# Kernel tuning notes

Measured on AMD Instinct MI355X. Metric: run time of the kernel, lower is better.

## Reference

```python
import jax, jax.numpy as jnp
import numpy as np

S, T, B = 50, 50, 64
SRC_V, TRG_V = 36616, 23262
E, EH, DH = 300, 512, 1024


def setup_inputs() -> dict:
    key = jax.random.key(0)
    ks = jax.random.split(key, 20)
    n = lambda k, shape: jax.random.normal(k, shape, jnp.float32) * 0.05
    return {
        "train_src_batch": jax.random.randint(ks[0], (S, B), 0, SRC_V),
        "train_trg_batch": jax.random.randint(ks[1], (T, B), 0, TRG_V),
        "emb_en": n(ks[2], (SRC_V, E)),
        "emb_de": n(ks[3], (TRG_V, E)),
        "enc_W_ih_f": n(ks[4], (4 * EH, E)),
        "enc_W_hh_f": n(ks[5], (4 * EH, EH)),
        "enc_b_f": n(ks[6], (4 * EH,)),
        "enc_W_ih_b": n(ks[7], (4 * EH, E)),
        "enc_W_hh_b": n(ks[8], (4 * EH, EH)),
        "enc_b_b": n(ks[9], (4 * EH,)),
        "dec_W_ih": n(ks[10], (4 * DH, E + DH)),
        "dec_W_hh": n(ks[11], (4 * DH, DH)),
        "dec_b": n(ks[12], (4 * DH,)),
        "W_gen": n(ks[13], (TRG_V, DH)),
        "b_gen": n(ks[14], (TRG_V,)),
        "W_i": n(ks[15], (DH, DH)),
        "W_o": n(ks[16], (DH, 2 * DH)),
    }


def _lstm_step(x, h, c, W_ih, W_hh, b):
    # PyTorch gate order: i, f, g, o
    gates = x @ W_ih.T + h @ W_hh.T + b
    i, f, g, o = jnp.split(gates, 4, axis=-1)
    c_new = jax.nn.sigmoid(f) * c + jax.nn.sigmoid(i) * jnp.tanh(g)
    h_new = jax.nn.sigmoid(o) * jnp.tanh(c_new)
    return h_new, c_new


def _run_lstm(x_seq, W_ih, W_hh, b, hidden):
    h0 = jnp.zeros((x_seq.shape[1], hidden), x_seq.dtype)
    def step(carry, x):
        h, c = carry
        h, c = _lstm_step(x, h, c, W_ih, W_hh, b)
        return (h, c), h
    (h, c), hs = jax.lax.scan(step, (h0, h0), x_seq)
    return hs, h, c


def _forward(train_src_batch, train_trg_batch, emb_en, emb_de,
             enc_W_ih_f, enc_W_hh_f, enc_b_f, enc_W_ih_b, enc_W_hh_b, enc_b_b,
             dec_W_ih, dec_W_hh, dec_b, W_gen, b_gen, W_i, W_o):
    x = emb_en[train_src_batch]                       # [S,B,E]
    hs_f, hf, cf = _run_lstm(x, enc_W_ih_f, enc_W_hh_f, enc_b_f, EH)
    hs_b, hb, cb = _run_lstm(x[::-1], enc_W_ih_b, enc_W_hh_b, enc_b_b, EH)
    output_hs = jnp.concatenate([hs_f, hs_b[::-1]], axis=-1)  # [S,B,1024]
    # Faithful to h.contiguous().view(B,1024) on direction-major [2,B,512]
    h = jnp.reshape(jnp.stack([hf, hb], axis=0), (B, DH))
    c = jnp.reshape(jnp.stack([cf, cb], axis=0), (B, DH))

    emb_trg = emb_de[train_trg_batch[: T - 1]]        # [T-1,B,E]

    def step(carry, e):
        h, c = carry
        # score[j,b] = output_hs[j,b] . (W_i h[b])  (the diag of the original mm)
        scores = jnp.einsum('sbd,bd->sb', output_hs, h @ W_i.T)
        # legacy nn.Softmax() on 2D input -> softmax over dim=1 (batch axis)
        a = jax.nn.softmax(scores, axis=1)
        s_t = jnp.einsum('sb,sbd->bd', a, output_hs)
        c_t = jnp.tanh(jnp.concatenate([s_t, h], axis=1) @ W_o.T)
        dec_in = jnp.concatenate([c_t, e], axis=1)    # [B, 1024+300]
        h, c = _lstm_step(dec_in, h, c, dec_W_ih, dec_W_hh, dec_b)
        logp = jax.nn.log_softmax(h @ W_gen.T + b_gen, axis=1)
        return (h, c), logp

    _, outs = jax.lax.scan(step, (h, c), emb_trg)     # [T-1,B,V]
    out0 = jnp.zeros((1, B, TRG_V), outs.dtype)       # output[0] filled with 0
    return jnp.concatenate([out0, outs], axis=0)      # [T,B,V]


def reference(train_src_batch, train_trg_batch, emb_en, emb_de,
              enc_W_ih_f, enc_W_hh_f, enc_b_f, enc_W_ih_b, enc_W_hh_b, enc_b_b,
              dec_W_ih, dec_W_hh, dec_b, W_gen, b_gen, W_i, W_o):
    return _forward(train_src_batch, train_trg_batch, emb_en, emb_de,
                    enc_W_ih_f, enc_W_hh_f, enc_b_f, enc_W_ih_b, enc_W_hh_b, enc_b_b,
                    dec_W_ih, dec_W_hh, dec_b, W_gen, b_gen, W_i, W_o)
```

## Files before the change

kernel.cpp:

```cpp
#include <hip/hip_runtime.h>
#include <hip/hip_bf16.h>

#define SS 50
#define TT 50
#define BB 64
#define TRGV 23262
#define EE 300
#define EH 512
#define DH 1024

#define GMRE 3136
#define GMP 3200
#define GK 1024
#define GNRE TRGV
#define GNP 23296

typedef short bf16x8 __attribute__((ext_vector_type(8)));
typedef float f32x4 __attribute__((ext_vector_type(4)));

__device__ __forceinline__ void glds16(const void* g, void* l) {
  __builtin_amdgcn_global_load_lds(
      (const __attribute__((address_space(1))) void*)g,
      (__attribute__((address_space(3))) void*)l, 16, 0, 0);
}

__device__ __forceinline__ float sigm(float x) { return 1.f / (1.f + expf(-x)); }
__device__ __forceinline__ float sum4(f32x4 v) { return v[0] + v[1] + v[2] + v[3]; }

__device__ __forceinline__ void split2(float x, __hip_bfloat16& hi, __hip_bfloat16& lo) {
  hi = __float2bfloat16(x);
  lo = __float2bfloat16(x - __bfloat162float(hi));
}

__device__ __forceinline__ void gbarg(unsigned* arrive, unsigned* gen,
                                      int idxInGrp, int n, bool poller) {
  __syncthreads();
  unsigned g = __hip_atomic_load(gen, __ATOMIC_RELAXED, __HIP_MEMORY_SCOPE_AGENT);
  if (threadIdx.x == 0)
    __hip_atomic_store(arrive + idxInGrp, g + 1u, __ATOMIC_RELEASE, __HIP_MEMORY_SCOPE_AGENT);
  if (poller) {
    int i = threadIdx.x;
    if (i < n) {
      while (__hip_atomic_load(arrive + i, __ATOMIC_RELAXED, __HIP_MEMORY_SCOPE_AGENT) < g + 1u)
        __builtin_amdgcn_s_sleep(1);
      (void)__hip_atomic_load(arrive + i, __ATOMIC_ACQUIRE, __HIP_MEMORY_SCOPE_AGENT);
    }
    __syncthreads();
    if (threadIdx.x == 0)
      __hip_atomic_store(gen, g + 1u, __ATOMIC_RELEASE, __HIP_MEMORY_SCOPE_AGENT);
  }
  if (threadIdx.x == 0) {
    while (__hip_atomic_load(gen, __ATOMIC_RELAXED, __HIP_MEMORY_SCOPE_AGENT) < g + 1u)
      __builtin_amdgcn_s_sleep(1);
    (void)__hip_atomic_load(gen, __ATOMIC_ACQUIRE, __HIP_MEMORY_SCOPE_AGENT);
  }
  __syncthreads();
}

__global__ void k_zero(float* __restrict__ p, long n) {
  long i = (long)blockIdx.x * 256 + threadIdx.x;
  if (i < n) p[i] = 0.f;
}
__global__ void k_zero_bf(__hip_bfloat16* __restrict__ p, long n) {
  long i = (long)blockIdx.x * 256 + threadIdx.x;
  if (i < n) p[i] = __float2bfloat16(0.f);
}

__global__ void k_embed(const int* __restrict__ src, const float* __restrict__ emb,
                        float* __restrict__ x) {
  int id = blockIdx.x * 256 + threadIdx.x;
  if (id >= SS * BB * EE) return;
  int sb = id / EE, e = id % EE;
  x[id] = emb[(long)src[sb] * EE + e];
}

__global__ void k_dbperm(const float* __restrict__ db, float* __restrict__ dbp) {
  int id = blockIdx.x * 256 + threadIdx.x;
  if (id >= 4096) return;
  int u = id >> 2, g = id & 3;
  dbp[id] = db[g * 1024 + u];
}

__global__ void k_split_pad(const float* __restrict__ in, int ld_in, int col_off,
                            int Kreal, int Kpad, int rows_real, long rows_pad,
                            int mode, __hip_bfloat16* __restrict__ out) {
  long id = (long)blockIdx.x * 256 + threadIdx.x;
  if (id >= rows_pad * Kpad) return;
  long r = id / Kpad;
  int k = id % Kpad;
  float v = 0.f;
  if (r < rows_real && k < Kreal) {
    if (mode == 3) {
      v = in[(long)k * ld_in + col_off + r];
    } else {
      long sr = r;
      if (mode == 1) sr = ((49 - (r >> 6)) << 6) + (r & 63);
      else if (mode == 2) sr = (long)(r & 3) * 1024 + (r >> 2);
      v = in[sr * ld_in + col_off + k];
    }
  }
  __hip_bfloat16 hi, lo;
  split2(v, hi, lo);
  out[r * 2 * Kpad + k] = hi;
  out[r * 2 * Kpad + Kpad + k] = lo;
}

__global__ void k_embgather_split(const int* __restrict__ trg, const float* __restrict__ emb,
                                  __hip_bfloat16* __restrict__ out) {
  long id = (long)blockIdx.x * 256 + threadIdx.x;
  if (id >= 3200L * 320) return;
  long r = id / 320;
  int k = id % 320;
  int t = r >> 6, b = r & 63;
  float v = 0.f;
  if (t < TT - 1 && k < EE) v = emb[(long)trg[t * BB + b] * EE + k];
  __hip_bfloat16 hi, lo;
  split2(v, hi, lo);
  out[r * 640 + k] = hi;
  out[r * 640 + 320 + k] = lo;
}

__global__ void k_tobf16_pad(const float* __restrict__ W, __hip_bfloat16* __restrict__ Wb,
                             long nrow_real, long nrow_pad, int K) {
  long id = (long)blockIdx.x * 256 + threadIdx.x;
  if (id >= nrow_pad * K) return;
  long r = id / K;
  Wb[id] = __float2bfloat16(r < nrow_real ? W[id] : 0.f);
}

__global__ void k_repackT(const float* __restrict__ in, float* __restrict__ out) {
  long id = (long)blockIdx.x * 256 + threadIdx.x;
  if (id >= 3200L * 1024) return;
  long r = id >> 10;
  int n = id & 1023;
  out[((long)(n >> 2) * 3200 + r) * 4 + (n & 3)] = in[id];
}

__global__ void k_repackG(const float* __restrict__ in, float* __restrict__ out) {
  long id = (long)blockIdx.x * 256 + threadIdx.x;
  if (id >= 3200L * 1024) return;
  long b = id / 51200;
  long r = id % 51200;
  long s = r >> 10;
  int d = r & 1023;
  out[id] = in[((long)s * 64 + b) * 1024 + d];
}

template<int OUTBF>
__global__ __launch_bounds__(256) void k_gsplit(
    const __hip_bfloat16* __restrict__ A2, const __hip_bfloat16* __restrict__ W2,
    const float* __restrict__ bias, void* __restrict__ Cout,
    int Mreal, int Nreal, int ldc, int Kpad) {
  __shared__ __hip_bfloat16 As[128 * 32];
  __shared__ __hip_bfloat16 Bs[128 * 32];
  int tid = threadIdx.x, lane = tid & 63, w = tid >> 6;
  long m0 = (long)blockIdx.y * 128, n0 = (long)blockIdx.x * 128;
  int lda2 = 2 * Kpad;
  int srow = lane >> 2;
  int scol = (lane & 3) * 8;
  char* lA0 = (char*)As + w * 2048;
  char* lA1 = lA0 + 1024;
  char* lB0 = (char*)Bs + w * 2048;
  char* lB1 = lB0 + 1024;
  int wm = (w >> 1) * 64, wn = (w & 1) * 64;
  int fr = lane & 15;
  int kc = (lane >> 4) * 8;
  f32x4 acc[4][4] = {};

  for (int seg = 0; seg < 3; ++seg) {
    const __hip_bfloat16* Ab = A2 + (seg == 1 ? Kpad : 0);
    const __hip_bfloat16* Wb = W2 + (seg == 2 ? Kpad : 0);
    const __hip_bfloat16* gA0 = Ab + (m0 + w * 32 + srow) * (long)lda2 + scol;
    const __hip_bfloat16* gA1 = gA0 + 16L * lda2;
    const __hip_bfloat16* gB0 = Wb + (n0 + w * 32 + srow) * (long)lda2 + scol;
    const __hip_bfloat16* gB1 = gB0 + 16L * lda2;
    for (int kt = 0; kt < Kpad / 32; ++kt) {
      int k0 = kt * 32;
      glds16(gA0 + k0, lA0);
      glds16(gA1 + k0, lA1);
      glds16(gB0 + k0, lB0);
      glds16(gB1 + k0, lB1);
      __syncthreads();
      bf16x8 a[4], b[4];
      for (int mi = 0; mi < 4; ++mi)
        a[mi] = *(const bf16x8*)(As + (wm + mi * 16 + fr) * 32 + kc);
      for (int ni = 0; ni < 4; ++ni)
        b[ni] = *(const bf16x8*)(Bs + (wn + ni * 16 + fr) * 32 + kc);
      for (int mi = 0; mi < 4; ++mi)
        for (int ni = 0; ni < 4; ++ni)
          acc[mi][ni] = __builtin_amdgcn_mfma_f32_16x16x32_bf16(a[mi], b[ni], acc[mi][ni], 0, 0, 0);
      __syncthreads();
    }
  }

  for (int mi = 0; mi < 4; ++mi) {
    for (int ni = 0; ni < 4; ++ni) {
      int n = (int)n0 + wn + ni * 16 + (lane & 15);
      if (n >= Nreal) continue;
      float bv = bias ? bias[n] : 0.f;
      for (int r = 0; r < 4; ++r) {
        int m = (int)m0 + wm + mi * 16 + (lane >> 4) * 4 + r;
        if (m >= Mreal) continue;
        float v = acc[mi][ni][r] + bv;
        if (OUTBF) ((__hip_bfloat16*)Cout)[(long)m * ldc + n] = __float2bfloat16(v);
        else ((float*)Cout)[(long)m * ldc + n] = v;
      }
    }
  }
}

__global__ __launch_bounds__(512) void persist_enc(
    const float* __restrict__ xW_f, const float* __restrict__ xW_b,
    const float* __restrict__ Whf, const float* __restrict__ Whb,
    float* __restrict__ hs, float* hA, float* hB, float* hA2, float* hB2,
    float* __restrict__ cf, float* __restrict__ cb,
    float* __restrict__ hd0, float* __restrict__ hT0, float* __restrict__ cdD,
    __hip_bfloat16* __restrict__ x2A, unsigned* __restrict__ bar) {
  __shared__ float WL[16 * 516];
  int t = threadIdx.x;
  int blk = blockIdx.x;
  int dir = blk >> 7, bl = blk & 127;
  const float* Whh = dir ? Whb : Whf;
  const float* xWb0 = dir ? xW_b : xW_f;
  float* c = dir ? cb : cf;
  float* hp = dir ? hA2 : hA;
  float* hn = dir ? hB2 : hB;
  unsigned* arrG = bar + dir * 128;
  unsigned* genG = bar + 784 + dir * 16;
  unsigned* arrA = bar + 256;
  unsigned* genA = bar + 816;

  for (int idx = t; idx < 16 * 512; idx += 512) {
    int r = idx >> 9, k = idx & 511;
    int srcrow = (r & 3) * 512 + (bl * 4 + (r >> 2));
    WL[r * 516 + k] = Whh[(long)srcrow * 512 + k];
  }
  __syncthreads();

  int j = t & 15;
  int b0 = t >> 4, b1 = b0 + 32;
  int g = j & 3;
  int ju = bl * 4 + (j >> 2);
  int lbase = (t & 63) & ~3;
  const f32x4* wq = (const f32x4*)(WL + j * 516);

  for (int s = 0; s < SS; ++s) {
    const f32x4* h0q = (const f32x4*)(hp + b0 * 512);
    const f32x4* h1q = (const f32x4*)(hp + b1 * 512);
    f32x4 v0 = {0, 0, 0, 0}, v1 = {0, 0, 0, 0};
    for (int q = 0; q < 128; ++q) {
      f32x4 wv = wq[q];
      v0 += wv * h0q[q];
      v1 += wv * h1q[q];
    }
    const float* xW = xWb0 + (long)(s * BB) * 2048;
    float a0 = sum4(v0) + xW[b0 * 2048 + g * 512 + ju];
    float a1 = sum4(v1) + xW[b1 * 2048 + g * 512 + ju];
    float gi0 = __shfl(a0, lbase + 0), gf0 = __shfl(a0, lbase + 1);
    float gg0 = __shfl(a0, lbase + 2), go0 = __shfl(a0, lbase + 3);
    float gi1 = __shfl(a1, lbase + 0), gf1 = __shfl(a1, lbase + 1);
    float gg1 = __shfl(a1, lbase + 2), go1 = __shfl(a1, lbase + 3);
    if ((t & 3) == 0) {
      int hscol = dir ? (512 + ju) : ju;
      int srow = dir ? (SS - 1 - s) : s;
      long hsrow0 = (long)(srow * BB + b0) * DH + hscol;
      long hsrow1 = (long)(srow * BB + b1) * DH + hscol;
      float cn0 = sigm(gf0) * c[b0 * 512 + ju] + sigm(gi0) * tanhf(gg0);
      float hn0 = sigm(go0) * tanhf(cn0);
      c[b0 * 512 + ju] = cn0;
      hn[b0 * 512 + ju] = hn0;
      hs[hsrow0] = hn0;
      float cn1 = sigm(gf1) * c[b1 * 512 + ju] + sigm(gi1) * tanhf(gg1);
      float hn1 = sigm(go1) * tanhf(cn1);
      c[b1 * 512 + ju] = cn1;
      hn[b1 * 512 + ju] = hn1;
      hs[hsrow1] = hn1;
    }
    float* tmp = hp; hp = hn; hn = tmp;
    gbarg(arrG, genG, bl, 128, bl == 0);
  }
  gbarg(arrA, genA, blk, 256, blk == 0);
  int gid = blk * 512 + t;
  if (gid < 65536) {
    int d2 = gid >> 15, b = (gid >> 9) & 63, j2 = gid & 511;
    float hv = (d2 ? hA2 : hA)[b * 512 + j2];
    float cv = (d2 ? cb : cf)[b * 512 + j2];
    hd0[gid] = hv;
    cdD[gid] = cv;
    int bp = gid >> 10, jp = gid & 1023;
    hT0[jp * 64 + bp] = hv;
    __hip_bfloat16 hi, lo;
    split2(hv, hi, lo);
    x2A[bp * 4096 + 1024 + jp] = hi;
    x2A[bp * 4096 + 3072 + jp] = lo;
  }
}

__global__ __launch_bounds__(1024) void persist_dec(
    const float* __restrict__ Gb, const float* __restrict__ HsWo1T,
    const float* __restrict__ Wo, const float* __restrict__ dWih,
    const float* __restrict__ dWhh, const __hip_bfloat16* __restrict__ Eg,
    float* hd0, float* hd1, float* hT0, float* hT1,
    float* __restrict__ cd, float* __restrict__ scoresG,
    __hip_bfloat16* __restrict__ A_bf,
    __hip_bfloat16* __restrict__ xA, __hip_bfloat16* __restrict__ xB,
    unsigned* __restrict__ bar) {
  __shared__ __hip_bfloat16 WB[16 * 4096];
  __shared__ float Abuf[4096];
  int t = threadIdx.x;
  int blk = blockIdx.x;
  int w = t >> 6, lane = t & 63;
  unsigned* arrive = bar + 512;
  unsigned* gen = bar + 832;

  for (int idx = t; idx < 16 * 2048; idx += 1024) {
    int jj = idx >> 11;
    int k = idx & 2047;
    int rp2 = blk * 16 + jj;
    long srcrow = (long)(rp2 & 3) * 1024 + (rp2 >> 2);
    float v = (k < 1024) ? dWih[srcrow * 1324 + k] : dWhh[srcrow * 1024 + (k - 1024)];
    __hip_bfloat16 hi, lo;
    split2(v, hi, lo);
    WB[((k >> 3) * 16 + jj) * 8 + (k & 7)] = hi;
    WB[(((k + 2048) >> 3) * 16 + jj) * 8 + (k & 7)] = lo;
  }
  __syncthreads();

  float* hcur = hd0; float* hnew = hd1;
  float* hTc = hT0;  float* hTn = hT1;
  int j = t & 15, b = t >> 4;
  int rp = blk * 16 + j;
  int ju = blk * 4 + (j >> 2);
  int lbase = (t & 63) & ~3;
  const f32x4* hw4 = (const f32x4*)(HsWo1T + (long)blk * 3200 * 4);
  f32x4* Abuf4 = (f32x4*)Abuf;
  int mt = w & 3, kg = w >> 2;
  int row_a = mt * 16 + (lane & 15), kq = lane >> 4;
  int s_ks = t >> 8, s_kq = (t >> 6) & 3, s_row = t & 63;
  const float* wo2 = Wo + (long)(blk * 4) * 2048 + 1024;

  for (int ts = 0; ts < TT - 1; ++ts) {
    const __hip_bfloat16* xc = (ts & 1) ? xB : xA;
    __hip_bfloat16* xn = (ts & 1) ? xA : xB;
    float eg = __bfloat162float(Eg[((long)(ts * BB + b)) * 4096 + rp]);

    if (blk < BB) {
      int sp = t >> 4, cc = t & 15;
      if (sp < SS) {
        const f32x4* gq = (const f32x4*)(Gb + (long)blk * 51200 + sp * 1024 + cc * 64);
        const f32x4* hq = (const f32x4*)(hcur + blk * DH + cc * 64);
        f32x4 a4 = {0, 0, 0, 0};
        #pragma unroll
        for (int q = 0; q < 16; ++q) a4 += gq[q] * hq[q];
        float p = sum4(a4);
        p += __shfl_xor(p, 1);
        p += __shfl_xor(p, 2);
        p += __shfl_xor(p, 4);
        p += __shfl_xor(p, 8);
        if (cc == 0) scoresG[sp * 64 + blk] = p;
      }
    }
    {
      f32x4 z1 = {0, 0, 0, 0};
      for (int k = w * 64; k < w * 64 + 64; ++k) {
        float hb = hTc[k * 64 + lane];
        f32x4 wv = {wo2[k], wo2[2048 + k], wo2[4096 + k], wo2[6144 + k]};
        z1 += hb * wv;
      }
      Abuf4[w * 64 + lane] = z1;
    }
    gbarg(arrive, gen, blk, 256, blk == 0);

    {
      f32x4 z2 = {0, 0, 0, 0};
      for (int s = w; s < SS; s += 16) {
        float sc = scoresG[s * 64 + lane];
        float m = sc;
        for (int o = 32; o > 0; o >>= 1) m = fmaxf(m, __shfl_xor(m, o));
        float e = expf(sc - m);
        float su = e;
        for (int o = 32; o > 0; o >>= 1) su += __shfl_xor(su, o);
        z2 += (e / su) * hw4[s * 64 + lane];
      }
      Abuf4[w * 64 + lane] += z2;
      __syncthreads();
      if (t < 256) {
        int bb = t >> 2, nl = t & 3;
        float sv = 0.f;
        for (int i = 0; i < 16; ++i) sv += Abuf[(i * 64 + bb) * 4 + nl];
        float ct = tanhf(sv);
        __hip_bfloat16 hi, lo;
        split2(ct, hi, lo);
        xn = xn;
        ((__hip_bfloat16*)xc)[bb * 4096 + blk * 4 + nl] = hi;
        ((__hip_bfloat16*)xc)[bb * 4096 + 2048 + blk * 4 + nl] = lo;
      }
    }
    gbarg(arrive, gen, blk, 256, blk == 0);

    {
      f32x4 acc = {0, 0, 0, 0};
      for (int seg = 0; seg < 3; ++seg) {
        int aoff = (seg == 1) ? 2048 : 0;
        int woff = (seg == 2) ? 2048 : 0;
        for (int c = 0; c < 16; ++c) {
          int k0 = c * 128;
          glds16(xc + (long)s_row * 4096 + aoff + k0 + s_ks * 32 + s_kq * 8,
                 (char*)Abuf + t * 16);
          __syncthreads();
          bf16x8 a = *(const bf16x8*)((__hip_bfloat16*)Abuf + kg * 2048 + kq * 512 + row_a * 8);
          int gidx = ((woff + k0 + kg * 32) >> 3) + kq;
          bf16x8 bfr = *(const bf16x8*)(WB + gidx * 128 + (lane & 15) * 8);
          acc = __builtin_amdgcn_mfma_f32_16x16x32_bf16(a, bfr, acc, 0, 0, 0);
          __syncthreads();
        }
      }
      for (int r = 0; r < 4; ++r) {
        int row = mt * 16 + kq * 4 + r;
        Abuf[kg * 1024 + row * 16 + (lane & 15)] = acc[r];
      }
      __syncthreads();
      float gv = Abuf[t] + Abuf[1024 + t] + Abuf[2048 + t] + Abuf[3072 + t] + eg;
      float gi0 = __shfl(gv, lbase + 0), gf0 = __shfl(gv, lbase + 1);
      float gg0 = __shfl(gv, lbase + 2), go0 = __shfl(gv, lbase + 3);
      if ((t & 3) == 0) {
        float cn0 = sigm(gf0) * cd[b * DH + ju] + sigm(gi0) * tanhf(gg0);
        float hn0 = sigm(go0) * tanhf(cn0);
        cd[b * DH + ju] = cn0;
        hnew[b * DH + ju] = hn0;
        hTn[ju * 64 + b] = hn0;
        __hip_bfloat16 hi, lo;
        split2(hn0, hi, lo);
        A_bf[(long)ts * (BB * DH) + b * DH + ju] = hi;
        xn[b * 4096 + 1024 + ju] = hi;
        xn[b * 4096 + 3072 + ju] = lo;
      }
    }
    { float* x = hcur; hcur = hnew; hnew = x; }
    { float* x = hTc; hTc = hTn; hTn = x; }
    gbarg(arrive, gen, blk, 256, blk == 0);
  }
}

__global__ __launch_bounds__(256) void k_gen_mfma(
    const __hip_bfloat16* __restrict__ A, const __hip_bfloat16* __restrict__ Bw,
    const float* __restrict__ bias, float* __restrict__ C) {
  __shared__ __hip_bfloat16 As[128 * 32];
  __shared__ __hip_bfloat16 Bs[128 * 32];
  int tid = threadIdx.x;
  int lane = tid & 63, w = tid >> 6;
  long m0 = (long)blockIdx.y * 128, n0 = (long)blockIdx.x * 128;
  int srow = lane >> 2;
  int scol = (lane & 3) * 8;
  const __hip_bfloat16* gA0 = A + (m0 + w * 32 + srow) * GK + scol;
  const __hip_bfloat16* gA1 = gA0 + 16 * GK;
  const __hip_bfloat16* gB0 = Bw + (n0 + w * 32 + srow) * GK + scol;
  const __hip_bfloat16* gB1 = gB0 + 16 * GK;
  char* lA0 = (char*)As + w * 2048;
  char* lA1 = lA0 + 1024;
  char* lB0 = (char*)Bs + w * 2048;
  char* lB1 = lB0 + 1024;
  int wm = (w >> 1) * 64, wn = (w & 1) * 64;
  int fr = lane & 15;
  int kc = (lane >> 4) * 8;
  f32x4 acc[4][4] = {};
  for (int kt = 0; kt < GK / 32; ++kt) {
    int k0 = kt * 32;
    glds16(gA0 + k0, lA0);
    glds16(gA1 + k0, lA1);
    glds16(gB0 + k0, lB0);
    glds16(gB1 + k0, lB1);
    __syncthreads();
    bf16x8 a[4], b[4];
    for (int mi = 0; mi < 4; ++mi)
      a[mi] = *(const bf16x8*)(As + (wm + mi * 16 + fr) * 32 + kc);
    for (int ni = 0; ni < 4; ++ni)
      b[ni] = *(const bf16x8*)(Bs + (wn + ni * 16 + fr) * 32 + kc);
    for (int mi = 0; mi < 4; ++mi)
      for (int ni = 0; ni < 4; ++ni)
        acc[mi][ni] = __builtin_amdgcn_mfma_f32_16x16x32_bf16(a[mi], b[ni], acc[mi][ni], 0, 0, 0);
    __syncthreads();
  }
  for (int mi = 0; mi < 4; ++mi) {
    for (int ni = 0; ni < 4; ++ni) {
      int n = (int)n0 + wn + ni * 16 + (lane & 15);
      if (n >= GNRE) continue;
      float bv = bias[n];
      for (int r = 0; r < 4; ++r) {
        int m = (int)m0 + wm + mi * 16 + (lane >> 4) * 4 + r;
        if (m < GMRE) C[(long)m * TRGV + n] = acc[mi][ni][r] + bv;
      }
    }
  }
}

__global__ __launch_bounds__(256) void k_logsoftmax(float* __restrict__ out) {
  int r = blockIdx.x;
  float* p = out + (long)(BB + r) * TRGV;
  int tid = threadIdx.x;
  __shared__ float red[256];
  float m = -1e30f;
  for (int i = tid; i < TRGV; i += 256) m = fmaxf(m, p[i]);
  red[tid] = m;
  __syncthreads();
  for (int s = 128; s > 0; s >>= 1) {
    if (tid < s) red[tid] = fmaxf(red[tid], red[tid + s]);
    __syncthreads();
  }
  m = red[0];
  __syncthreads();
  float sum = 0.f;
  for (int i = tid; i < TRGV; i += 256) sum += expf(p[i] - m);
  red[tid] = sum;
  __syncthreads();
  for (int s = 128; s > 0; s >>= 1) {
    if (tid < s) red[tid] += red[tid + s];
    __syncthreads();
  }
  float lse = m + logf(red[0]);
  for (int i = tid; i < TRGV; i += 256) p[i] -= lse;
}

extern "C" void kernel_launch(void* const* d_in, const int* in_sizes, int n_in,
                              void* d_out, int out_size, void* d_ws, size_t ws_size,
                              hipStream_t stream) {
  const int* src = (const int*)d_in[0];
  const int* trg = (const int*)d_in[1];
  const float* emb_en = (const float*)d_in[2];
  const float* emb_de = (const float*)d_in[3];
  const float* eWih_f = (const float*)d_in[4];
  const float* eWhh_f = (const float*)d_in[5];
  const float* eb_f = (const float*)d_in[6];
  const float* eWih_b = (const float*)d_in[7];
  const float* eWhh_b = (const float*)d_in[8];
  const float* eb_b = (const float*)d_in[9];
  const float* dWih = (const float*)d_in[10];
  const float* dWhh = (const float*)d_in[11];
  const float* db = (const float*)d_in[12];
  const float* Wgen = (const float*)d_in[13];
  const float* bgen = (const float*)d_in[14];
  const float* Wi = (const float*)d_in[15];
  const float* Wo = (const float*)d_in[16];
  float* out = (float*)d_out;

  float* base = (float*)d_ws;
  __hip_bfloat16* xsf = (__hip_bfloat16*)base;
  __hip_bfloat16* xsb = (__hip_bfloat16*)(base + 1024000);
  __hip_bfloat16* Wihf2 = (__hip_bfloat16*)(base + 2048000);
  __hip_bfloat16* Wihb2 = (__hip_bfloat16*)(base + 2703360);
  float* xW_f = base + 3358720;
  float* xW_b = base + 9912320;
  __hip_bfloat16* hs2 = (__hip_bfloat16*)base;
  __hip_bfloat16* Wi2 = (__hip_bfloat16*)(base + 3276800);
  __hip_bfloat16* Wo12 = (__hip_bfloat16*)(base + 4325376);
  __hip_bfloat16* eg2 = (__hip_bfloat16*)(base + 5373952);
  __hip_bfloat16* Wce2 = (__hip_bfloat16*)(base + 6397952);
  __hip_bfloat16* E_g = (__hip_bfloat16*)(base + 7708672);
  __hip_bfloat16* Wgen_bf = (__hip_bfloat16*)base;
  float* p = base + 16465920;
  float* x_enc = p; p += SS * BB * EE;
  float* hs = p; p += (long)SS * BB * DH;
  float* G = p; p += (long)SS * BB * DH;
  float* Gb = p; p += (long)SS * BB * DH;
  float* HsWo1 = p; p += (long)SS * BB * DH;
  float* HsWo1T = p; p += (long)SS * BB * DH;
  __hip_bfloat16* A_bf = (__hip_bfloat16*)p; p += (GMP * GK) / 2;
  __hip_bfloat16* x2A = (__hip_bfloat16*)p; p += (BB * 4096) / 2;
  __hip_bfloat16* x2B = (__hip_bfloat16*)p; p += (BB * 4096) / 2;
  float* dbp = p; p += 4096;
  float* scoresG = p; p += SS * BB;
  float* hd0 = p; p += BB * DH;
  float* hd1 = p; p += BB * DH;
  float* hT0 = p; p += BB * DH;
  float* hT1 = p; p += BB * DH;
  float* cd = p; p += BB * DH;
  float* hA = p; p += BB * EH;
  float* hB = p; p += BB * EH;
  float* hA2 = p; p += BB * EH;
  float* hB2 = p; p += BB * EH;
  float* cf = p; p += BB * EH;
  float* cb = p; p += BB * EH;
  unsigned* bar = (unsigned*)p; p += 1024;

  dim3 b256(256);

  k_embed<<<dim3((SS * BB * EE + 255) / 256), b256, 0, stream>>>(src, emb_en, x_enc);
  k_zero<<<dim3((6 * BB * EH + 255) / 256), b256, 0, stream>>>(hA, 6 * BB * EH);
  k_zero<<<dim3(4), b256, 0, stream>>>((float*)bar, 1024);
  k_zero<<<dim3((int)(((long)BB * TRGV + 255) / 256)), b256, 0, stream>>>(out, (long)BB * TRGV);
  k_zero_bf<<<dim3(((GMP - GMRE) * GK + 255) / 256), b256, 0, stream>>>(
      A_bf + (long)GMRE * GK, (long)(GMP - GMRE) * GK);
  k_dbperm<<<dim3(16), b256, 0, stream>>>(db, dbp);

  k_split_pad<<<dim3((3200 * 320 + 255) / 256), b256, 0, stream>>>(
      x_enc, EE, 0, EE, 320, 3200, 3200, 0, xsf);
  k_split_pad<<<dim3((3200 * 320 + 255) / 256), b256, 0, stream>>>(
      x_enc, EE, 0, EE, 320, 3200, 3200, 1, xsb);
  k_split_pad<<<dim3((2048 * 320 + 255) / 256), b256, 0, stream>>>(
      eWih_f, EE, 0, EE, 320, 2048, 2048, 0, Wihf2);
  k_split_pad<<<dim3((2048 * 320 + 255) / 256), b256, 0, stream>>>(
      eWih_b, EE, 0, EE, 320, 2048, 2048, 0, Wihb2);
  k_gsplit<0><<<dim3(16, 25), b256, 0, stream>>>(xsf, Wihf2, eb_f, xW_f, 3200, 2048, 2048, 320);
  k_gsplit<0><<<dim3(16, 25), b256, 0, stream>>>(xsb, Wihb2, eb_b, xW_b, 3200, 2048, 2048, 320);

  {
    void* args[] = {(void*)&xW_f, (void*)&xW_b, (void*)&eWhh_f, (void*)&eWhh_b,
                    (void*)&hs, (void*)&hA, (void*)&hB, (void*)&hA2, (void*)&hB2,
                    (void*)&cf, (void*)&cb, (void*)&hd0, (void*)&hT0, (void*)&cd,
                    (void*)&x2A, (void*)&bar};
    hipLaunchCooperativeKernel((const void*)persist_enc, dim3(256), dim3(512),
                               args, 0, stream);
  }

  k_split_pad<<<dim3((int)((3200L * 1024 + 255) / 256)), b256, 0, stream>>>(
      hs, DH, 0, DH, 1024, 3200, 3200, 0, hs2);
  k_split_pad<<<dim3((int)((1024L * 1024 + 255) / 256)), b256, 0, stream>>>(
      Wi, DH, 0, DH, 1024, 1024, 1024, 3, Wi2);
  k_split_pad<<<dim3((int)((1024L * 1024 + 255) / 256)), b256, 0, stream>>>(
      Wo, 2 * DH, 0, DH, 1024, 1024, 1024, 0, Wo12);
  k_embgather_split<<<dim3((int)((3200L * 320 + 255) / 256)), b256, 0, stream>>>(
      trg, emb_de, eg2);
  k_split_pad<<<dim3((int)((4096L * 320 + 255) / 256)), b256, 0, stream>>>(
      dWih, 1324, 1024, EE, 320, 4096, 4096, 2, Wce2);
  k_gsplit<0><<<dim3(8, 25), b256, 0, stream>>>(hs2, Wi2, (const float*)nullptr, G, 3200, 1024, 1024, 1024);
  k_gsplit<0><<<dim3(8, 25), b256, 0, stream>>>(hs2, Wo12, (const float*)nullptr, HsWo1, 3200, 1024, 1024, 1024);
  k_repackG<<<dim3((int)((3200L * 1024 + 255) / 256)), b256, 0, stream>>>(G, Gb);
  k_repackT<<<dim3((int)((3200L * 1024 + 255) / 256)), b256, 0, stream>>>(HsWo1, HsWo1T);
  k_gsplit<1><<<dim3(32, 25), b256, 0, stream>>>(eg2, Wce2, dbp, E_g, 3136, 4096, 4096, 320);

  {
    void* args[] = {(void*)&Gb, (void*)&HsWo1T, (void*)&Wo, (void*)&dWih, (void*)&dWhh,
                    (void*)&E_g, (void*)&hd0, (void*)&hd1, (void*)&hT0, (void*)&hT1,
                    (void*)&cd, (void*)&scoresG, (void*)&A_bf, (void*)&x2A, (void*)&x2B,
                    (void*)&bar};
    hipLaunchCooperativeKernel((const void*)persist_dec, dim3(256), dim3(1024),
                               args, 0, stream);
  }

  k_tobf16_pad<<<dim3((int)(((long)GNP * GK + 255) / 256)), b256, 0, stream>>>(
      Wgen, Wgen_bf, GNRE, GNP, GK);
  k_gen_mfma<<<dim3(GNP / 128, GMP / 128), b256, 0, stream>>>(
      A_bf, Wgen_bf, bgen, out + (long)BB * TRGV);
  k_logsoftmax<<<dim3((TT - 1) * BB), b256, 0, stream>>>(out);
}
```

Measured before the change: 6.669 ms.

## Pad barrier slots, spread attention scores over 200 blocks, drop LDS staging in decoder GEMV

Barrier arrival counters are spaced 16 words apart so each block's flag sits on its own cache line, and the poller becomes the last block instead of block 0. Attention scores are now computed by 200 blocks, one wave per (s,b) pair, reading G directly, which removes the separate repackG kernel and its buffer. The decoder gate MFMA loop reads A fragments straight from global memory rather than staging them through LDS with two __syncthreads per chunk. The aim is to shorten the per-step critical path of the persistent decoder. The cost is uncoalesced-looking direct global A loads that depend on cache hits, and a larger barrier buffer.

```diff
diff --git a/kernel.cpp b/kernel.cpp
--- a/kernel.cpp
+++ b/kernel.cpp
@@ -37,13 +37,13 @@
   __syncthreads();
   unsigned g = __hip_atomic_load(gen, __ATOMIC_RELAXED, __HIP_MEMORY_SCOPE_AGENT);
   if (threadIdx.x == 0)
-    __hip_atomic_store(arrive + idxInGrp, g + 1u, __ATOMIC_RELEASE, __HIP_MEMORY_SCOPE_AGENT);
+    __hip_atomic_store(arrive + idxInGrp * 16, g + 1u, __ATOMIC_RELEASE, __HIP_MEMORY_SCOPE_AGENT);
   if (poller) {
     int i = threadIdx.x;
     if (i < n) {
-      while (__hip_atomic_load(arrive + i, __ATOMIC_RELAXED, __HIP_MEMORY_SCOPE_AGENT) < g + 1u)
+      while (__hip_atomic_load(arrive + i * 16, __ATOMIC_RELAXED, __HIP_MEMORY_SCOPE_AGENT) < g + 1u)
         __builtin_amdgcn_s_sleep(1);
-      (void)__hip_atomic_load(arrive + i, __ATOMIC_ACQUIRE, __HIP_MEMORY_SCOPE_AGENT);
+      (void)__hip_atomic_load(arrive + i * 16, __ATOMIC_ACQUIRE, __HIP_MEMORY_SCOPE_AGENT);
     }
     __syncthreads();
     if (threadIdx.x == 0)
@@ -134,16 +134,6 @@
   long r = id >> 10;
   int n = id & 1023;
   out[((long)(n >> 2) * 3200 + r) * 4 + (n & 3)] = in[id];
-}
-
-__global__ void k_repackG(const float* __restrict__ in, float* __restrict__ out) {
-  long id = (long)blockIdx.x * 256 + threadIdx.x;
-  if (id >= 3200L * 1024) return;
-  long b = id / 51200;
-  long r = id % 51200;
-  long s = r >> 10;
-  int d = r & 1023;
-  out[id] = in[((long)s * 64 + b) * 1024 + d];
 }
 
 template<int OUTBF>
@@ -225,10 +215,10 @@
   float* c = dir ? cb : cf;
   float* hp = dir ? hA2 : hA;
   float* hn = dir ? hB2 : hB;
-  unsigned* arrG = bar + dir * 128;
-  unsigned* genG = bar + 784 + dir * 16;
-  unsigned* arrA = bar + 256;
-  unsigned* genA = bar + 816;
+  unsigned* arrG = bar + dir * 2048;
+  unsigned* genG = bar + 12288 + dir * 16;
+  unsigned* arrA = bar + 4096;
+  unsigned* genA = bar + 12320;
 
   for (int idx = t; idx < 16 * 512; idx += 512) {
     int r = idx >> 9, k = idx & 511;
@@ -297,7 +287,7 @@
 }
 
 __global__ __launch_bounds__(1024) void persist_dec(
-    const float* __restrict__ Gb, const float* __restrict__ HsWo1T,
+    const float* __restrict__ G, const float* __restrict__ HsWo1T,
     const float* __restrict__ Wo, const float* __restrict__ dWih,
     const float* __restrict__ dWhh, const __hip_bfloat16* __restrict__ Eg,
     float* hd0, float* hd1, float* hT0, float* hT1,
@@ -305,13 +295,14 @@
     __hip_bfloat16* __restrict__ A_bf,
     __hip_bfloat16* __restrict__ xA, __hip_bfloat16* __restrict__ xB,
     unsigned* __restrict__ bar) {
-  __shared__ __hip_bfloat16 WB[16 * 4096];
+  __shared__ __hip_bfloat16 WB[512 * 128];
   __shared__ float Abuf[4096];
   int t = threadIdx.x;
   int blk = blockIdx.x;
   int w = t >> 6, lane = t & 63;
-  unsigned* arrive = bar + 512;
-  unsigned* gen = bar + 832;
+  unsigned* arrive = bar + 8192;
+  unsigned* gen = bar + 12336;
+  bool pol = (blk == 255);
 
   for (int idx = t; idx < 16 * 2048; idx += 1024) {
     int jj = idx >> 11;
@@ -331,34 +322,31 @@
   int j = t & 15, b = t >> 4;
   int rp = blk * 16 + j;
   int ju = blk * 4 + (j >> 2);
-  int lbase = (t & 63) & ~3;
+  int lbase = lane & ~3;
   const f32x4* hw4 = (const f32x4*)(HsWo1T + (long)blk * 3200 * 4);
   f32x4* Abuf4 = (f32x4*)Abuf;
+  const float* wo2 = Wo + (long)(blk * 4) * 2048 + 1024;
   int mt = w & 3, kg = w >> 2;
-  int row_a = mt * 16 + (lane & 15), kq = lane >> 4;
-  int s_ks = t >> 8, s_kq = (t >> 6) & 3, s_row = t & 63;
-  const float* wo2 = Wo + (long)(blk * 4) * 2048 + 1024;
+  int row_a = mt * 16 + (lane & 15);
+  int kq = lane >> 4;
 
   for (int ts = 0; ts < TT - 1; ++ts) {
     const __hip_bfloat16* xc = (ts & 1) ? xB : xA;
     __hip_bfloat16* xn = (ts & 1) ? xA : xB;
     float eg = __bfloat162float(Eg[((long)(ts * BB + b)) * 4096 + rp]);
 
-    if (blk < BB) {
-      int sp = t >> 4, cc = t & 15;
-      if (sp < SS) {
-        const f32x4* gq = (const f32x4*)(Gb + (long)blk * 51200 + sp * 1024 + cc * 64);
-        const f32x4* hq = (const f32x4*)(hcur + blk * DH + cc * 64);
-        f32x4 a4 = {0, 0, 0, 0};
-        #pragma unroll
-        for (int q = 0; q < 16; ++q) a4 += gq[q] * hq[q];
-        float p = sum4(a4);
-        p += __shfl_xor(p, 1);
-        p += __shfl_xor(p, 2);
-        p += __shfl_xor(p, 4);
-        p += __shfl_xor(p, 8);
-        if (cc == 0) scoresG[sp * 64 + blk] = p;
-      }
+    if (blk < 200) {
+      int s = blk >> 2;
+      int bb = (blk & 3) * 16 + (t >> 6);
+      int ln = t & 63;
+      const f32x4* gq = (const f32x4*)(G + ((long)s * 64 + bb) * 1024);
+      const f32x4* hq = (const f32x4*)(hcur + bb * 1024);
+      f32x4 a4 = {0, 0, 0, 0};
+      #pragma unroll
+      for (int q = 0; q < 4; ++q) a4 += gq[ln + q * 64] * hq[ln + q * 64];
+      float p = sum4(a4);
+      for (int o = 1; o < 64; o <<= 1) p += __shfl_xor(p, o);
+      if (ln == 0) scoresG[s * 64 + bb] = p;
     }
     {
       f32x4 z1 = {0, 0, 0, 0};
@@ -369,7 +357,7 @@
       }
       Abuf4[w * 64 + lane] = z1;
     }
-    gbarg(arrive, gen, blk, 256, blk == 0);
+    gbarg(arrive, gen, blk, 256, pol);
 
     {
       f32x4 z2 = {0, 0, 0, 0};
@@ -391,34 +379,29 @@
         float ct = tanhf(sv);
         __hip_bfloat16 hi, lo;
         split2(ct, hi, lo);
-        xn = xn;
         ((__hip_bfloat16*)xc)[bb * 4096 + blk * 4 + nl] = hi;
         ((__hip_bfloat16*)xc)[bb * 4096 + 2048 + blk * 4 + nl] = lo;
       }
     }
-    gbarg(arrive, gen, blk, 256, blk == 0);
+    gbarg(arrive, gen, blk, 256, pol);
 
     {
       f32x4 acc = {0, 0, 0, 0};
+      const __hip_bfloat16* xrow = xc + (long)row_a * 4096 + kq * 8;
       for (int seg = 0; seg < 3; ++seg) {
         int aoff = (seg == 1) ? 2048 : 0;
         int woff = (seg == 2) ? 2048 : 0;
+        #pragma unroll
         for (int c = 0; c < 16; ++c) {
-          int k0 = c * 128;
-          glds16(xc + (long)s_row * 4096 + aoff + k0 + s_ks * 32 + s_kq * 8,
-                 (char*)Abuf + t * 16);
-          __syncthreads();
-          bf16x8 a = *(const bf16x8*)((__hip_bfloat16*)Abuf + kg * 2048 + kq * 512 + row_a * 8);
-          int gidx = ((woff + k0 + kg * 32) >> 3) + kq;
-          bf16x8 bfr = *(const bf16x8*)(WB + gidx * 128 + (lane & 15) * 8);
+          int kb = kg * 512 + c * 32;
+          bf16x8 a = *(const bf16x8*)(xrow + aoff + kb);
+          int gidx = ((woff + kb) >> 3) + kq;
+          bf16x8 bfr = *(const bf16x8*)(WB + (gidx * 16 + (lane & 15)) * 8);
           acc = __builtin_amdgcn_mfma_f32_16x16x32_bf16(a, bfr, acc, 0, 0, 0);
-          __syncthreads();
         }
       }
-      for (int r = 0; r < 4; ++r) {
-        int row = mt * 16 + kq * 4 + r;
-        Abuf[kg * 1024 + row * 16 + (lane & 15)] = acc[r];
-      }
+      for (int r = 0; r < 4; ++r)
+        Abuf[kg * 1024 + (mt * 16 + kq * 4 + r) * 16 + (lane & 15)] = acc[r];
       __syncthreads();
       float gv = Abuf[t] + Abuf[1024 + t] + Abuf[2048 + t] + Abuf[3072 + t] + eg;
       float gi0 = __shfl(gv, lbase + 0), gf0 = __shfl(gv, lbase + 1);
@@ -438,7 +421,7 @@
     }
     { float* x = hcur; hcur = hnew; hnew = x; }
     { float* x = hTc; hTc = hTn; hTn = x; }
-    gbarg(arrive, gen, blk, 256, blk == 0);
+    gbarg(arrive, gen, blk, 256, pol);
   }
 }
 
@@ -561,7 +544,6 @@
   float* x_enc = p; p += SS * BB * EE;
   float* hs = p; p += (long)SS * BB * DH;
   float* G = p; p += (long)SS * BB * DH;
-  float* Gb = p; p += (long)SS * BB * DH;
   float* HsWo1 = p; p += (long)SS * BB * DH;
   float* HsWo1T = p; p += (long)SS * BB * DH;
   __hip_bfloat16* A_bf = (__hip_bfloat16*)p; p += (GMP * GK) / 2;
@@ -580,13 +562,13 @@
   float* hB2 = p; p += BB * EH;
   float* cf = p; p += BB * EH;
   float* cb = p; p += BB * EH;
-  unsigned* bar = (unsigned*)p; p += 1024;
+  unsigned* bar = (unsigned*)p; p += 12352;
 
   dim3 b256(256);
 
   k_embed<<<dim3((SS * BB * EE + 255) / 256), b256, 0, stream>>>(src, emb_en, x_enc);
   k_zero<<<dim3((6 * BB * EH + 255) / 256), b256, 0, stream>>>(hA, 6 * BB * EH);
-  k_zero<<<dim3(4), b256, 0, stream>>>((float*)bar, 1024);
+  k_zero<<<dim3(49), b256, 0, stream>>>((float*)bar, 12352);
   k_zero<<<dim3((int)(((long)BB * TRGV + 255) / 256)), b256, 0, stream>>>(out, (long)BB * TRGV);
   k_zero_bf<<<dim3(((GMP - GMRE) * GK + 255) / 256), b256, 0, stream>>>(
       A_bf + (long)GMRE * GK, (long)(GMP - GMRE) * GK);
@@ -624,12 +606,11 @@
       dWih, 1324, 1024, EE, 320, 4096, 4096, 2, Wce2);
   k_gsplit<0><<<dim3(8, 25), b256, 0, stream>>>(hs2, Wi2, (const float*)nullptr, G, 3200, 1024, 1024, 1024);
   k_gsplit<0><<<dim3(8, 25), b256, 0, stream>>>(hs2, Wo12, (const float*)nullptr, HsWo1, 3200, 1024, 1024, 1024);
-  k_repackG<<<dim3((int)((3200L * 1024 + 255) / 256)), b256, 0, stream>>>(G, Gb);
   k_repackT<<<dim3((int)((3200L * 1024 + 255) / 256)), b256, 0, stream>>>(HsWo1, HsWo1T);
   k_gsplit<1><<<dim3(32, 25), b256, 0, stream>>>(eg2, Wce2, dbp, E_g, 3136, 4096, 4096, 320);
 
   {
-    void* args[] = {(void*)&Gb, (void*)&HsWo1T, (void*)&Wo, (void*)&dWih, (void*)&dWhh,
+    void* args[] = {(void*)&G, (void*)&HsWo1T, (void*)&Wo, (void*)&dWih, (void*)&dWhh,
                     (void*)&E_g, (void*)&hd0, (void*)&hd1, (void*)&hT0, (void*)&hT1,
                     (void*)&cd, (void*)&scoresG, (void*)&A_bf, (void*)&x2A, (void*)&x2B,
                     (void*)&bar};
```

Measured after the change: 6.431 ms. 3.6% less time.
